# Kernel tuning notes

Measured on AMD Instinct MI355X. Metric: run time of the kernel, lower is better.

The kernel has to match this reference:

```python
import jax, jax.numpy as jnp
import numpy as np

MAX_DIST = 5
D_PE = 16
NUM_ENTITIES = 50000
NUM_EDGES = 800000
NUM_ANCHOR_TRIPLES = 32
MAX_SOURCES = 2 * NUM_ANCHOR_TRIPLES  # upper bound on unique anchor entities


def setup_inputs() -> dict:
    key = jax.random.key(0)
    k1, k2, k3, k4 = jax.random.split(key, 4)
    h_ids = jax.random.randint(k1, (NUM_EDGES,), 0, NUM_ENTITIES)
    t_ids = jax.random.randint(k2, (NUM_EDGES,), 0, NUM_ENTITIES)
    anchor_triple_indices = jax.random.randint(k3, (NUM_ANCHOR_TRIPLES,), 0, NUM_EDGES)
    dist_embed = jax.random.normal(k4, (MAX_DIST + 1, D_PE), dtype=jnp.float32)
    return {
        "h_ids": h_ids,
        "t_ids": t_ids,
        "anchor_triple_indices": anchor_triple_indices,
        "num_entities": NUM_ENTITIES,
        "dist_embed": dist_embed,
    }


def _bfs_mean_counts(h_ids, t_ids, anchor_triple_indices, num_entities):
    """Returns [num_entities, MAX_DIST+1] mean one-hot distance counts over anchors."""
    # unique anchor entities, padded with -1 to a static size (torch.unique equivalent)
    anchor_ents = jnp.concatenate([h_ids[anchor_triple_indices], t_ids[anchor_triple_indices]])
    sources = jnp.unique(anchor_ents, size=MAX_SOURCES, fill_value=-1)  # [K], sorted
    valid = sources >= 0                                                # [K]
    src = jnp.where(valid, sources, 0)
    K = src.shape[0]
    col = jnp.arange(K)

    # symmetric adjacency as edge list (duplicates are harmless: only >0 is tested)
    edge_src = jnp.concatenate([h_ids, t_ids])  # [2E]
    edge_dst = jnp.concatenate([t_ids, h_ids])  # [2E]

    frontier = jnp.zeros((num_entities, K), jnp.float32).at[src, col].set(1.0)
    visited = jnp.zeros((num_entities, K), bool).at[src, col].set(True)
    dist = jnp.full((num_entities, K), MAX_DIST, jnp.int32).at[src, col].set(0)

    for depth in range(1, MAX_DIST + 1):  # fixed small hop count
        # sparse adj @ frontier == scatter-add of gathered frontier rows
        new_frontier = jax.ops.segment_sum(frontier[edge_src], edge_dst, num_segments=num_entities)
        newly = (new_frontier > 0) & ~visited
        dist = jnp.where(newly, depth, dist)
        visited = visited | newly
        frontier = newly.astype(jnp.float32)

    # masked mean over valid anchor sources, expressed as distance-count histogram
    w = valid.astype(jnp.float32)
    n_valid = jnp.maximum(w.sum(), 1.0)
    onehot = jax.nn.one_hot(dist, MAX_DIST + 1, dtype=jnp.float32)  # [N, K, D+1]
    counts = jnp.einsum('nkd,k->nd', onehot, w) / n_valid           # [N, D+1]
    return counts


def reference(h_ids, t_ids, anchor_triple_indices, num_entities, dist_embed):
    counts = _bfs_mean_counts(h_ids, t_ids, anchor_triple_indices, num_entities)
    # mean over sources of embed(dist) == counts @ embedding table
    return counts @ dist_embed  # [num_entities, d_pe]
```

## Files before the change

### kernel.cpp

```cpp
#include <hip/hip_runtime.h>
#include <hip/hip_bf16.h>

typedef unsigned long long u64;
typedef unsigned int u32;
typedef unsigned short u16;

#define MAXD 5
#define BSH  6
#define BN   64
#define NW   1024
#define NTH  256
#define CAPG 2816
#define HEMPTY 0xFFFFFFFFu


__global__ __launch_bounds__(NTH) void chunk_sort(
    const int* __restrict__ h, const int* __restrict__ t, int E, int CE, int CAPC,
    int NB, u32* __restrict__ recs, u16* __restrict__ segtab,
    const int* __restrict__ anchor, int A,
    u64* __restrict__ NFg, u32* __restrict__ srcPack, int* __restrict__ nvalid) {
    extern __shared__ u32 sh[];
    u32* buf   = sh;
    u32* offs  = buf + CAPC;
    u32* cur   = offs + NB;
    u32* hsKey = cur + NB;
    u32* hsBit = hsKey + 128;
    u32* waveSum = hsBit + 128;
    int tid = threadIdx.x, c = blockIdx.x;
    int lane = tid & 63, w = tid >> 6;
    int lo = c * CE, hi = min(E, lo + CE);
    int ne = hi - lo;
    int nrec = 2 * ne;

    for (int i = tid; i < NB; i += NTH) cur[i] = 0u;
    if (tid < 128) hsKey[tid] = HEMPTY;
    __syncthreads();

    if (tid < 64) {
        int K = 2 * A;
        int a_ = (tid < K) ? anchor[(tid < A) ? tid : (tid - A)] : 0;
        int my = (tid < K) ? ((tid < A) ? h[a_] : t[a_]) : -1;
        bool uniq = (tid < K);
        for (int j = 0; j < 64; ++j) {
            int o = __shfl(my, j, 64);
            if (j < tid && o == my) uniq = false;
        }
        u64 mask = __ballot(uniq);
        if (c == 0 && tid == 0) *nvalid = (int)__popcll(mask);
        if (uniq) {
            u32 slot = ((u32)my * 2654435761u) >> 25;
            while (atomicCAS(&hsKey[slot], HEMPTY, (u32)my) != HEMPTY)
                slot = (slot + 1) & 127u;
            hsBit[slot] = (u32)tid;
        }
        if (c == 0)
            srcPack[tid] = uniq ? (((u32)my << BSH) | (u32)tid) : HEMPTY;
    }

    for (int i = tid; i < ne; i += NTH) {
        u32 uu = (u32)h[lo + i], vv = (u32)t[lo + i];
        atomicAdd(&cur[vv >> BSH], 1u);
        atomicAdd(&cur[uu >> BSH], 1u);
    }
    __syncthreads();

    {
        u32 i0 = (u32)tid * 4;
        u32 aa[4];
#pragma unroll
        for (int k = 0; k < 4; ++k) {
            u32 i = i0 + k;
            aa[k] = (i < (u32)NB) ? cur[i] : 0u;
        }
        u32 sum = aa[0] + aa[1] + aa[2] + aa[3];
        u32 p = sum;
#pragma unroll
        for (int d = 1; d < 64; d <<= 1) {
            u32 x = (u32)__shfl_up((int)p, d, 64);
            if (lane >= d) p += x;
        }
        u32 excl = p - sum;
        if (lane == 63) waveSum[w] = p;
        __syncthreads();
        u32 woff = 0;
        for (int k = 0; k < w; ++k) woff += waveSum[k];
        u32 o0 = woff + excl;
        u32 oo[4] = {o0, o0 + aa[0], o0 + aa[0] + aa[1],
                     o0 + aa[0] + aa[1] + aa[2]};
#pragma unroll
        for (int k = 0; k < 4; ++k) {
            u32 i = i0 + k;
            if (i < (u32)NB) {
                offs[i] = oo[k];
                segtab[c * (NB + 1) + i] = (u16)oo[k];
                cur[i] = 0u;
            }
        }
        if (tid == 0) segtab[c * (NB + 1) + NB] = (u16)nrec;
    }
    __syncthreads();

    auto srcMask = [&](u32 src) -> u64 {
        u32 slot = (src * 2654435761u) >> 25;
        while (true) {
            u32 k = hsKey[slot];
            if (k == src) return 1ull << hsBit[slot];
            if (k == HEMPTY) return 0ull;
            slot = (slot + 1) & 127u;
        }
    };

    for (int i = tid; i < ne; i += NTH) {
        u32 uu = (u32)h[lo + i], vv = (u32)t[lo + i];
        u32 b1 = vv >> BSH;
        buf[offs[b1] + atomicAdd(&cur[b1], 1u)] = (uu << BSH) | (vv & (BN - 1));
        u32 b2 = uu >> BSH;
        buf[offs[b2] + atomicAdd(&cur[b2], 1u)] = (vv << BSH) | (uu & (BN - 1));
        if (uu != vv) {
            u64 m1 = srcMask(uu);
            if (m1) atomicOr(&NFg[vv], m1);
            u64 m2 = srcMask(vv);
            if (m2) atomicOr(&NFg[uu], m2);
        }
    }
    __syncthreads();
    for (int i = tid; i < nrec; i += NTH) recs[c * CAPC + i] = buf[i];
}

__global__ __launch_bounds__(NTH) void level12_merge(
    const u32* __restrict__ recs, const u16* __restrict__ segtab, int CAPC, int NB,
    const u32* __restrict__ srcPack, const u64* __restrict__ NFg,
    u64* __restrict__ F2, u64* __restrict__ V, u64* __restrict__ CNT,
    u32* __restrict__ recs2, u32* __restrict__ bucketCnt, int N) {
    __shared__ u16 s0a[NW];
    __shared__ u32 loff[NW + 1];
    __shared__ u32 waveSum[4];
    __shared__ u32 buf[CAPG];
    __shared__ u64 NF[BN];
    __shared__ u32 srcL[64];
    int b = blockIdx.x, tid = threadIdx.x;
    int lane = tid & 63, w = tid >> 6;
    if (tid < BN) NF[tid] = 0ull;
    if (tid < 64) srcL[tid] = srcPack[tid];

    u32 c0 = (u32)tid * 4;
    u32 aa[4], ll[4];
#pragma unroll
    for (int k = 0; k < 4; ++k) {
        u32 c = c0 + k;
        u32 a = segtab[c * (NB + 1) + b];
        u32 e = segtab[c * (NB + 1) + b + 1];
        s0a[c] = (u16)a;
        aa[k] = a;
        ll[k] = e - a;
    }
    u32 sum = ll[0] + ll[1] + ll[2] + ll[3];
    u32 p = sum;
#pragma unroll
    for (int d = 1; d < 64; d <<= 1) {
        u32 x = (u32)__shfl_up((int)p, d, 64);
        if (lane >= d) p += x;
    }
    u32 excl = p - sum;
    if (lane == 63) waveSum[w] = p;
    __syncthreads();
    u32 woff = 0;
    for (int k = 0; k < w; ++k) woff += waveSum[k];
    u32 base = woff + excl;
    loff[c0]     = base;
    loff[c0 + 1] = base + ll[0];
    loff[c0 + 2] = base + ll[0] + ll[1];
    loff[c0 + 3] = base + ll[0] + ll[1] + ll[2];
    if (tid == NTH - 1) loff[NW] = base + sum;
    (void)aa;
    __syncthreads();

    u32 T = min(loff[NW], (u32)CAPG);

    u32 per = (T + NTH - 1) / NTH;
    u32 j0 = min((u32)tid * per, T), j1 = min(j0 + per, T);
    if (j0 < j1) {
        int c = 0;
#pragma unroll
        for (int step = 512; step >= 1; step >>= 1)
            if (c + step <= NW - 1 && loff[c + step] <= j0) c += step;
        for (u32 j = j0; j < j1; ++j) {
            while (loff[c + 1] <= j) ++c;
            buf[j] = recs[(u32)c * CAPC + (u32)s0a[c] + (j - loff[c])];
        }
    }
    __syncthreads();

    u32 o0 = (u32)b * CAPG;
    u32 r = tid;
    for (; r + 3u * NTH < T; r += 4u * NTH) {
        u32 r0 = buf[r],           r1 = buf[r + NTH];
        u32 r2 = buf[r + 2 * NTH], r3 = buf[r + 3 * NTH];
        recs2[o0 + r] = r0;
        recs2[o0 + r + NTH] = r1;
        recs2[o0 + r + 2 * NTH] = r2;
        recs2[o0 + r + 3 * NTH] = r3;
        u64 f0 = NFg[r0 >> BSH], f1 = NFg[r1 >> BSH];
        u64 f2 = NFg[r2 >> BSH], f3 = NFg[r3 >> BSH];
        if (f0) atomicOr(&NF[r0 & (BN - 1)], f0);
        if (f1) atomicOr(&NF[r1 & (BN - 1)], f1);
        if (f2) atomicOr(&NF[r2 & (BN - 1)], f2);
        if (f3) atomicOr(&NF[r3 & (BN - 1)], f3);
    }
    for (; r < T; r += NTH) {
        u32 r0 = buf[r];
        recs2[o0 + r] = r0;
        u64 f0 = NFg[r0 >> BSH];
        if (f0) atomicOr(&NF[r0 & (BN - 1)], f0);
    }
    __syncthreads();
    if (tid == 0) bucketCnt[b] = T;
    if (tid < BN) {
        int n = b * BN + tid;
        if (n < N) {
            u64 srcbit = 0ull;
            for (int k = 0; k < 64; ++k) {
                u32 pk = srcL[k];
                if (pk != HEMPTY && (int)(pk >> BSH) == n)
                    srcbit |= 1ull << (pk & (BN - 1));
            }
            u64 nf1 = NFg[n];
            u64 v1 = srcbit | nf1;
            u64 newly2 = NF[tid] & ~v1;
            V[n] = v1 | newly2;
            F2[n] = newly2;
            CNT[n] = (srcbit ? 1ull : 0ull)
                   | ((u64)__popcll(nf1) << 8)
                   | ((u64)__popcll(newly2) << 16);
        }
    }
}

__global__ __launch_bounds__(NTH) void level3(
    const u32* __restrict__ recs2, const u32* __restrict__ bucketCnt,
    const u64* __restrict__ Fin, u64* __restrict__ Fout,
    u64* __restrict__ V, u64* __restrict__ CNT, int N) {
    __shared__ u64 NF[BN];
    int b = blockIdx.x, tid = threadIdx.x;
    u32 o0 = (u32)b * CAPG;
    u32 cnt = bucketCnt[b];
    if (tid < BN) NF[tid] = 0ull;
    __syncthreads();
    u32 r = tid;
    for (; r + 3u * NTH < cnt; r += 4u * NTH) {
        u32 c0 = recs2[o0 + r],           c1 = recs2[o0 + r + NTH];
        u32 c2 = recs2[o0 + r + 2 * NTH], c3 = recs2[o0 + r + 3 * NTH];
        u64 f0 = Fin[c0 >> BSH], f1 = Fin[c1 >> BSH];
        u64 f2 = Fin[c2 >> BSH], f3 = Fin[c3 >> BSH];
        if (f0) atomicOr(&NF[c0 & (BN - 1)], f0);
        if (f1) atomicOr(&NF[c1 & (BN - 1)], f1);
        if (f2) atomicOr(&NF[c2 & (BN - 1)], f2);
        if (f3) atomicOr(&NF[c3 & (BN - 1)], f3);
    }
    for (; r < cnt; r += NTH) {
        u32 c0 = recs2[o0 + r];
        u64 f0 = Fin[c0 >> BSH];
        if (f0) atomicOr(&NF[c0 & (BN - 1)], f0);
    }
    __syncthreads();
    if (tid < BN) {
        int n = b * BN + tid;
        if (n < N) {
            u64 vis = V[n];
            u64 newly = NF[tid] & ~vis;
            Fout[n] = newly;
            if (newly) {
                V[n] = vis | newly;
                CNT[n] += (u64)__popcll(newly) << 24;
            }
        }
    }
}

__global__ __launch_bounds__(NTH) void level4_fin(
    const u32* __restrict__ recs2, const u32* __restrict__ bucketCnt,
    const u64* __restrict__ Fin, const u64* __restrict__ V,
    const u64* __restrict__ CNT, const int* __restrict__ nvalid,
    const float* __restrict__ embed, float* __restrict__ out, int N) {
    __shared__ u64 NF[BN];
    int b = blockIdx.x, tid = threadIdx.x;
    u32 o0 = (u32)b * CAPG;
    u32 cnt = bucketCnt[b];
    if (tid < BN) NF[tid] = 0ull;
    __syncthreads();
    u32 r = tid;
    for (; r + 3u * NTH < cnt; r += 4u * NTH) {
        u32 c0 = recs2[o0 + r],           c1 = recs2[o0 + r + NTH];
        u32 c2 = recs2[o0 + r + 2 * NTH], c3 = recs2[o0 + r + 3 * NTH];
        u64 f0 = Fin[c0 >> BSH], f1 = Fin[c1 >> BSH];
        u64 f2 = Fin[c2 >> BSH], f3 = Fin[c3 >> BSH];
        if (f0) atomicOr(&NF[c0 & (BN - 1)], f0);
        if (f1) atomicOr(&NF[c1 & (BN - 1)], f1);
        if (f2) atomicOr(&NF[c2 & (BN - 1)], f2);
        if (f3) atomicOr(&NF[c3 & (BN - 1)], f3);
    }
    for (; r < cnt; r += NTH) {
        u32 c0 = recs2[o0 + r];
        u64 f0 = Fin[c0 >> BSH];
        if (f0) atomicOr(&NF[c0 & (BN - 1)], f0);
    }
    __syncthreads();
    int nl = tid >> 2, q = tid & 3;
    int n = b * BN + nl;
    if (n >= N) return;
    u64 vis = V[n];
    int c4 = __popcll(NF[nl] & ~vis);
    u64 c = CNT[n];
    int nv = *nvalid;
    float inv = 1.0f / (float)(nv > 0 ? nv : 1);
    float cd[MAXD + 1];
    int total = c4;
#pragma unroll
    for (int d = 0; d < 4; ++d) {
        int x = (int)((c >> (8 * d)) & 0xffull);
        total += x;
        cd[d] = (float)x;
    }
    cd[4] = (float)c4;
    cd[5] = (float)(nv - total);

    const float4* e4 = (const float4*)embed;
    float4 acc = {0.f, 0.f, 0.f, 0.f};
#pragma unroll
    for (int d = 0; d <= MAXD; ++d) {
        float4 e = e4[d * 4 + q];
        acc.x += cd[d] * e.x; acc.y += cd[d] * e.y;
        acc.z += cd[d] * e.z; acc.w += cd[d] * e.w;
    }
    acc.x *= inv; acc.y *= inv; acc.z *= inv; acc.w *= inv;
    ((float4*)(out + (size_t)n * 16))[q] = acc;
}

extern "C" void kernel_launch(void* const* d_in, const int* in_sizes, int n_in,
                              void* d_out, int out_size, void* d_ws, size_t ws_size,
                              hipStream_t stream) {
    const int*   h      = (const int*)d_in[0];
    const int*   t      = (const int*)d_in[1];
    const int*   anchor = (const int*)d_in[2];
    const float* embed  = (const float*)d_in[4];
    float*       out    = (float*)d_out;

    int E = in_sizes[0];
    int A = in_sizes[2];
    int D = in_sizes[4] / (MAXD + 1);
    int N = out_size / D;
    int NB = (N + BN - 1) >> BSH;
    int CE = (E + NW - 1) / NW;
    int CAPC = 2 * CE;
    (void)D;

    u64* NFg = (u64*)d_ws;
    u64* V   = NFg + N;
    u64* CNT = V + N;
    u64* F2  = CNT + N;
    u64* F3  = F2 + N;
    u32* srcPack   = (u32*)(F3 + N);
    int* nvalid    = (int*)(srcPack + 64);
    u32* bucketCnt = (u32*)(nvalid + 1);
    u32* recs      = bucketCnt + NB;
    u16* segtab    = (u16*)(recs + (size_t)NW * CAPC);
    u32* recs2     = (u32*)(segtab + (size_t)NW * (NB + 1));

    hipMemsetAsync(NFg, 0, (size_t)N * 8, stream);

    size_t shmem = (size_t)(CAPC + 2 * NB + 260) * sizeof(u32);
    chunk_sort<<<NW, NTH, shmem, stream>>>(h, t, E, CE, CAPC, NB, recs, segtab,
                                           anchor, A, NFg, srcPack, nvalid);

    level12_merge<<<NB, NTH, 0, stream>>>(recs, segtab, CAPC, NB, srcPack, NFg,
                                          F2, V, CNT, recs2, bucketCnt, N);
    level3<<<NB, NTH, 0, stream>>>(recs2, bucketCnt, F2, F3, V, CNT, N);
    level4_fin<<<NB, NTH, 0, stream>>>(recs2, bucketCnt, F3, V, CNT,
                                       nvalid, embed, out, N);
}
```

Baseline: 135.2 us.

## Fuse BFS stages into one persistent kernel with grid-wide barriers

Merges the chunk sort, level-1/2 merge, level-3 and final level-4 kernels into a single launch. Stages are separated by a software grid barrier built on an atomic counter, and the NFg memset is moved into the kernel. Each block keeps its gathered bucket records, visited bits and counts in shared memory across levels, so the recs2, V, CNT and bucketCnt global round trips go away. The chunk count now equals the bucket count so all blocks can be co-resident. This risks deadlock if not every block is resident, and the barrier spin adds its own latency.

```diff
diff --git a/kernel.cpp b/kernel.cpp
--- a/kernel.cpp
+++ b/kernel.cpp
@@ -1,5 +1,4 @@
 #include <hip/hip_runtime.h>
-#include <hip/hip_bf16.h>
 
 typedef unsigned long long u64;
 typedef unsigned int u32;
@@ -8,71 +7,207 @@
 #define MAXD 5
 #define BSH  6
 #define BN   64
-#define NW   1024
 #define NTH  256
 #define CAPG 2816
+#define MAXC 1024
 #define HEMPTY 0xFFFFFFFFu
 
 
-__global__ __launch_bounds__(NTH) void chunk_sort(
+__device__ __forceinline__ void gbar(u32* bar, u32 target) {
+    __syncthreads();
+    if (threadIdx.x == 0) {
+        __threadfence();
+        atomicAdd(bar, 1u);
+        while (__hip_atomic_load(bar, __ATOMIC_RELAXED,
+                                 __HIP_MEMORY_SCOPE_AGENT) < target)
+            __builtin_amdgcn_s_sleep(2);
+        __threadfence();
+    }
+    __syncthreads();
+}
+
+__global__ __launch_bounds__(NTH, 4) void fused(
     const int* __restrict__ h, const int* __restrict__ t, int E, int CE, int CAPC,
     int NB, u32* __restrict__ recs, u16* __restrict__ segtab,
     const int* __restrict__ anchor, int A,
-    u64* __restrict__ NFg, u32* __restrict__ srcPack, int* __restrict__ nvalid) {
+    u64* __restrict__ NFg, u32* __restrict__ srcPack, int* __restrict__ nvalid,
+    u32* __restrict__ bar,
+    u64* __restrict__ F2g, u64* __restrict__ F3g,
+    const float* __restrict__ embed, float* __restrict__ out, int N) {
     extern __shared__ u32 sh[];
-    u32* buf   = sh;
-    u32* offs  = buf + CAPC;
-    u32* cur   = offs + NB;
-    u32* hsKey = cur + NB;
-    u32* hsBit = hsKey + 128;
-    u32* waveSum = hsBit + 128;
-    int tid = threadIdx.x, c = blockIdx.x;
-    int lane = tid & 63, w = tid >> 6;
-    int lo = c * CE, hi = min(E, lo + CE);
-    int ne = hi - lo;
-    int nrec = 2 * ne;
-
-    for (int i = tid; i < NB; i += NTH) cur[i] = 0u;
-    if (tid < 128) hsKey[tid] = HEMPTY;
-    __syncthreads();
-
-    if (tid < 64) {
-        int K = 2 * A;
-        int a_ = (tid < K) ? anchor[(tid < A) ? tid : (tid - A)] : 0;
-        int my = (tid < K) ? ((tid < A) ? h[a_] : t[a_]) : -1;
-        bool uniq = (tid < K);
-        for (int j = 0; j < 64; ++j) {
-            int o = __shfl(my, j, 64);
-            if (j < tid && o == my) uniq = false;
-        }
-        u64 mask = __ballot(uniq);
-        if (c == 0 && tid == 0) *nvalid = (int)__popcll(mask);
-        if (uniq) {
-            u32 slot = ((u32)my * 2654435761u) >> 25;
-            while (atomicCAS(&hsKey[slot], HEMPTY, (u32)my) != HEMPTY)
+    const int tid = threadIdx.x;
+    const int b = blockIdx.x;
+    const int lane = tid & 63, w = tid >> 6;
+    const u32 nb = (u32)gridDim.x;
+
+    u32* buf2 = sh;
+    u64* NF   = (u64*)(sh + CAPG);
+    u64* Vl   = NF + BN;
+    u64* CNTl = Vl + BN;
+    u32* scr  = (u32*)(CNTl + BN);
+    u16* s0a  = (u16*)scr;
+    u32* loff = scr + MAXC / 2;
+    u32* wS2  = loff + MAXC + 1;
+    u32* srcL = wS2 + 4;
+
+    { int i = b * NTH + tid; if (i < N) NFg[i] = 0ull; }
+    gbar(bar, nb);
+
+    {
+        u32* cbuf  = sh;
+        u32* offs  = cbuf + CAPC;
+        u32* cur   = offs + NB;
+        u32* hsKey = cur + NB;
+        u32* hsBit = hsKey + 128;
+        u32* wS    = hsBit + 128;
+        int lo = b * CE, hi = min(E, lo + CE);
+        int ne = hi - lo, nrec = 2 * ne;
+
+        for (int i = tid; i < NB; i += NTH) cur[i] = 0u;
+        if (tid < 128) hsKey[tid] = HEMPTY;
+        __syncthreads();
+
+        if (tid < 64) {
+            int K = 2 * A;
+            int a_ = (tid < K) ? anchor[(tid < A) ? tid : (tid - A)] : 0;
+            int my = (tid < K) ? ((tid < A) ? h[a_] : t[a_]) : -1;
+            bool uniq = (tid < K);
+            for (int j = 0; j < 64; ++j) {
+                int o = __shfl(my, j, 64);
+                if (j < tid && o == my) uniq = false;
+            }
+            u64 mask = __ballot(uniq);
+            if (b == 0 && tid == 0) *nvalid = (int)__popcll(mask);
+            if (uniq) {
+                u32 slot = ((u32)my * 2654435761u) >> 25;
+                while (atomicCAS(&hsKey[slot], HEMPTY, (u32)my) != HEMPTY)
+                    slot = (slot + 1) & 127u;
+                hsBit[slot] = (u32)tid;
+            }
+            if (b == 0)
+                srcPack[tid] = uniq ? (((u32)my << BSH) | (u32)tid) : HEMPTY;
+        }
+
+        u32 eu[4], ev[4];
+#pragma unroll
+        for (int k = 0; k < 4; ++k) {
+            int i = tid + k * NTH;
+            u32 uu = 0u, vv = 0u;
+            if (i < ne) {
+                uu = (u32)h[lo + i]; vv = (u32)t[lo + i];
+                atomicAdd(&cur[vv >> BSH], 1u);
+                atomicAdd(&cur[uu >> BSH], 1u);
+            }
+            eu[k] = uu; ev[k] = vv;
+        }
+        for (int i = tid + 4 * NTH; i < ne; i += NTH) {
+            u32 uu = (u32)h[lo + i], vv = (u32)t[lo + i];
+            atomicAdd(&cur[vv >> BSH], 1u);
+            atomicAdd(&cur[uu >> BSH], 1u);
+        }
+        __syncthreads();
+
+        {
+            u32 i0 = (u32)tid * 4;
+            u32 aa[4];
+#pragma unroll
+            for (int k = 0; k < 4; ++k) {
+                u32 i = i0 + k;
+                aa[k] = (i < (u32)NB) ? cur[i] : 0u;
+            }
+            u32 sum = aa[0] + aa[1] + aa[2] + aa[3];
+            u32 p = sum;
+#pragma unroll
+            for (int d = 1; d < 64; d <<= 1) {
+                u32 x = (u32)__shfl_up((int)p, d, 64);
+                if (lane >= d) p += x;
+            }
+            u32 excl = p - sum;
+            if (lane == 63) wS[w] = p;
+            __syncthreads();
+            u32 woff = 0;
+            for (int k = 0; k < w; ++k) woff += wS[k];
+            u32 o0 = woff + excl;
+            u32 oo[4] = {o0, o0 + aa[0], o0 + aa[0] + aa[1],
+                         o0 + aa[0] + aa[1] + aa[2]};
+#pragma unroll
+            for (int k = 0; k < 4; ++k) {
+                u32 i = i0 + k;
+                if (i < (u32)NB) {
+                    offs[i] = oo[k];
+                    segtab[b * (NB + 1) + i] = (u16)oo[k];
+                    cur[i] = 0u;
+                }
+            }
+            if (tid == 0) segtab[b * (NB + 1) + NB] = (u16)nrec;
+        }
+        __syncthreads();
+
+        auto srcMask = [&](u32 src) -> u64 {
+            u32 slot = (src * 2654435761u) >> 25;
+            while (true) {
+                u32 k = hsKey[slot];
+                if (k == src) return 1ull << hsBit[slot];
+                if (k == HEMPTY) return 0ull;
                 slot = (slot + 1) & 127u;
-            hsBit[slot] = (u32)tid;
-        }
-        if (c == 0)
-            srcPack[tid] = uniq ? (((u32)my << BSH) | (u32)tid) : HEMPTY;
+            }
+        };
+
+#pragma unroll
+        for (int k = 0; k < 4; ++k) {
+            int i = tid + k * NTH;
+            if (i < ne) {
+                u32 uu = eu[k], vv = ev[k];
+                u32 b1 = vv >> BSH;
+                cbuf[offs[b1] + atomicAdd(&cur[b1], 1u)] = (uu << BSH) | (vv & (BN - 1));
+                u32 b2 = uu >> BSH;
+                cbuf[offs[b2] + atomicAdd(&cur[b2], 1u)] = (vv << BSH) | (uu & (BN - 1));
+                if (uu != vv) {
+                    u64 m1 = srcMask(uu);
+                    if (m1) atomicOr(&NFg[vv], m1);
+                    u64 m2 = srcMask(vv);
+                    if (m2) atomicOr(&NFg[uu], m2);
+                }
+            }
+        }
+        for (int i = tid + 4 * NTH; i < ne; i += NTH) {
+            u32 uu = (u32)h[lo + i], vv = (u32)t[lo + i];
+            u32 b1 = vv >> BSH;
+            cbuf[offs[b1] + atomicAdd(&cur[b1], 1u)] = (uu << BSH) | (vv & (BN - 1));
+            u32 b2 = uu >> BSH;
+            cbuf[offs[b2] + atomicAdd(&cur[b2], 1u)] = (vv << BSH) | (uu & (BN - 1));
+            if (uu != vv) {
+                u64 m1 = srcMask(uu);
+                if (m1) atomicOr(&NFg[vv], m1);
+                u64 m2 = srcMask(vv);
+                if (m2) atomicOr(&NFg[uu], m2);
+            }
+        }
+        __syncthreads();
+        for (int i = tid; i < nrec; i += NTH) recs[b * CAPC + i] = cbuf[i];
     }
-
-    for (int i = tid; i < ne; i += NTH) {
-        u32 uu = (u32)h[lo + i], vv = (u32)t[lo + i];
-        atomicAdd(&cur[vv >> BSH], 1u);
-        atomicAdd(&cur[uu >> BSH], 1u);
-    }
-    __syncthreads();
-
+    gbar(bar, 2 * nb);
+
+    u32 T;
     {
-        u32 i0 = (u32)tid * 4;
-        u32 aa[4];
+        if (tid < BN) NF[tid] = 0ull;
+        if (tid < 64) srcL[tid] = srcPack[tid];
+
+        u32 c0 = (u32)tid * 4;
+        u32 ll[4];
 #pragma unroll
         for (int k = 0; k < 4; ++k) {
-            u32 i = i0 + k;
-            aa[k] = (i < (u32)NB) ? cur[i] : 0u;
-        }
-        u32 sum = aa[0] + aa[1] + aa[2] + aa[3];
+            u32 c = c0 + k;
+            u32 l_ = 0u;
+            if (c < (u32)NB) {
+                u32 a = segtab[c * (NB + 1) + b];
+                u32 e = segtab[c * (NB + 1) + b + 1];
+                s0a[c] = (u16)a;
+                l_ = e - a;
+            }
+            ll[k] = l_;
+        }
+        u32 sum = ll[0] + ll[1] + ll[2] + ll[3];
         u32 p = sum;
 #pragma unroll
         for (int d = 1; d < 64; d <<= 1) {
@@ -80,260 +215,149 @@
             if (lane >= d) p += x;
         }
         u32 excl = p - sum;
-        if (lane == 63) waveSum[w] = p;
+        if (lane == 63) wS2[w] = p;
         __syncthreads();
         u32 woff = 0;
-        for (int k = 0; k < w; ++k) woff += waveSum[k];
-        u32 o0 = woff + excl;
-        u32 oo[4] = {o0, o0 + aa[0], o0 + aa[0] + aa[1],
-                     o0 + aa[0] + aa[1] + aa[2]};
-#pragma unroll
-        for (int k = 0; k < 4; ++k) {
-            u32 i = i0 + k;
-            if (i < (u32)NB) {
-                offs[i] = oo[k];
-                segtab[c * (NB + 1) + i] = (u16)oo[k];
-                cur[i] = 0u;
-            }
-        }
-        if (tid == 0) segtab[c * (NB + 1) + NB] = (u16)nrec;
+        for (int k = 0; k < w; ++k) woff += wS2[k];
+        u32 base = woff + excl;
+        loff[c0]     = base;
+        loff[c0 + 1] = base + ll[0];
+        loff[c0 + 2] = base + ll[0] + ll[1];
+        loff[c0 + 3] = base + ll[0] + ll[1] + ll[2];
+        if (tid == NTH - 1) loff[MAXC] = base + sum;
+        __syncthreads();
+        T = min(loff[MAXC], (u32)CAPG);
+
+        u32 per = (T + NTH - 1) / NTH;
+        u32 j0 = min((u32)tid * per, T), j1 = min(j0 + per, T);
+        if (j0 < j1) {
+            int c = 0;
+#pragma unroll
+            for (int step = 512; step >= 1; step >>= 1)
+                if (c + step <= MAXC - 1 && loff[c + step] <= j0) c += step;
+            for (u32 j = j0; j < j1; ++j) {
+                while (loff[c + 1] <= j) ++c;
+                buf2[j] = recs[(u32)c * CAPC + (u32)s0a[c] + (j - loff[c])];
+            }
+        }
+        __syncthreads();
+
+        u32 r = tid;
+        for (; r + 3u * NTH < T; r += 4u * NTH) {
+            u32 r0 = buf2[r],           r1 = buf2[r + NTH];
+            u32 r2 = buf2[r + 2 * NTH], r3 = buf2[r + 3 * NTH];
+            u64 f0 = NFg[r0 >> BSH], f1 = NFg[r1 >> BSH];
+            u64 f2 = NFg[r2 >> BSH], f3 = NFg[r3 >> BSH];
+            if (f0) atomicOr(&NF[r0 & (BN - 1)], f0);
+            if (f1) atomicOr(&NF[r1 & (BN - 1)], f1);
+            if (f2) atomicOr(&NF[r2 & (BN - 1)], f2);
+            if (f3) atomicOr(&NF[r3 & (BN - 1)], f3);
+        }
+        for (; r < T; r += NTH) {
+            u32 r0 = buf2[r];
+            u64 f0 = NFg[r0 >> BSH];
+            if (f0) atomicOr(&NF[r0 & (BN - 1)], f0);
+        }
+        __syncthreads();
+        if (tid < BN) {
+            int n = b * BN + tid;
+            u64 v2 = 0ull, cnt = 0ull;
+            if (n < N) {
+                u64 srcbit = 0ull;
+                for (int k = 0; k < 64; ++k) {
+                    u32 pk = srcL[k];
+                    if (pk != HEMPTY && (int)(pk >> BSH) == n)
+                        srcbit |= 1ull << (pk & (BN - 1));
+                }
+                u64 nf1 = NFg[n];
+                u64 v1 = srcbit | nf1;
+                u64 newly2 = NF[tid] & ~v1;
+                v2 = v1 | newly2;
+                F2g[n] = newly2;
+                cnt = (srcbit ? 1ull : 0ull)
+                    | ((u64)__popcll(nf1) << 8)
+                    | ((u64)__popcll(newly2) << 16);
+            }
+            Vl[tid] = v2;
+            CNTl[tid] = cnt;
+        }
     }
-    __syncthreads();
-
-    auto srcMask = [&](u32 src) -> u64 {
-        u32 slot = (src * 2654435761u) >> 25;
-        while (true) {
-            u32 k = hsKey[slot];
-            if (k == src) return 1ull << hsBit[slot];
-            if (k == HEMPTY) return 0ull;
-            slot = (slot + 1) & 127u;
+    gbar(bar, 3 * nb);
+
+    auto depth_pass = [&](const u64* __restrict__ Fin) {
+        u32 r = tid;
+        for (; r + 3u * NTH < T; r += 4u * NTH) {
+            u32 r0 = buf2[r],           r1 = buf2[r + NTH];
+            u32 r2 = buf2[r + 2 * NTH], r3 = buf2[r + 3 * NTH];
+            u64 f0 = Fin[r0 >> BSH], f1 = Fin[r1 >> BSH];
+            u64 f2 = Fin[r2 >> BSH], f3 = Fin[r3 >> BSH];
+            if (f0) atomicOr(&NF[r0 & (BN - 1)], f0);
+            if (f1) atomicOr(&NF[r1 & (BN - 1)], f1);
+            if (f2) atomicOr(&NF[r2 & (BN - 1)], f2);
+            if (f3) atomicOr(&NF[r3 & (BN - 1)], f3);
+        }
+        for (; r < T; r += NTH) {
+            u32 r0 = buf2[r];
+            u64 f0 = Fin[r0 >> BSH];
+            if (f0) atomicOr(&NF[r0 & (BN - 1)], f0);
         }
     };
 
-    for (int i = tid; i < ne; i += NTH) {
-        u32 uu = (u32)h[lo + i], vv = (u32)t[lo + i];
-        u32 b1 = vv >> BSH;
-        buf[offs[b1] + atomicAdd(&cur[b1], 1u)] = (uu << BSH) | (vv & (BN - 1));
-        u32 b2 = uu >> BSH;
-        buf[offs[b2] + atomicAdd(&cur[b2], 1u)] = (vv << BSH) | (uu & (BN - 1));
-        if (uu != vv) {
-            u64 m1 = srcMask(uu);
-            if (m1) atomicOr(&NFg[vv], m1);
-            u64 m2 = srcMask(vv);
-            if (m2) atomicOr(&NFg[uu], m2);
+    {
+        if (tid < BN) NF[tid] = 0ull;
+        __syncthreads();
+        depth_pass(F2g);
+        __syncthreads();
+        if (tid < BN) {
+            int n = b * BN + tid;
+            if (n < N) {
+                u64 vis = Vl[tid];
+                u64 newly = NF[tid] & ~vis;
+                F3g[n] = newly;
+                if (newly) {
+                    Vl[tid] = vis | newly;
+                    CNTl[tid] += (u64)__popcll(newly) << 24;
+                }
+            }
         }
     }
-    __syncthreads();
-    for (int i = tid; i < nrec; i += NTH) recs[c * CAPC + i] = buf[i];
-}
-
-__global__ __launch_bounds__(NTH) void level12_merge(
-    const u32* __restrict__ recs, const u16* __restrict__ segtab, int CAPC, int NB,
-    const u32* __restrict__ srcPack, const u64* __restrict__ NFg,
-    u64* __restrict__ F2, u64* __restrict__ V, u64* __restrict__ CNT,
-    u32* __restrict__ recs2, u32* __restrict__ bucketCnt, int N) {
-    __shared__ u16 s0a[NW];
-    __shared__ u32 loff[NW + 1];
-    __shared__ u32 waveSum[4];
-    __shared__ u32 buf[CAPG];
-    __shared__ u64 NF[BN];
-    __shared__ u32 srcL[64];
-    int b = blockIdx.x, tid = threadIdx.x;
-    int lane = tid & 63, w = tid >> 6;
-    if (tid < BN) NF[tid] = 0ull;
-    if (tid < 64) srcL[tid] = srcPack[tid];
-
-    u32 c0 = (u32)tid * 4;
-    u32 aa[4], ll[4];
-#pragma unroll
-    for (int k = 0; k < 4; ++k) {
-        u32 c = c0 + k;
-        u32 a = segtab[c * (NB + 1) + b];
-        u32 e = segtab[c * (NB + 1) + b + 1];
-        s0a[c] = (u16)a;
-        aa[k] = a;
-        ll[k] = e - a;
+    gbar(bar, 4 * nb);
+
+    {
+        if (tid < BN) NF[tid] = 0ull;
+        __syncthreads();
+        depth_pass(F3g);
+        __syncthreads();
+        int nl = tid >> 2, q = tid & 3;
+        int n = b * BN + nl;
+        if (n >= N) return;
+        u64 vis = Vl[nl];
+        int c4 = __popcll(NF[nl] & ~vis);
+        u64 c = CNTl[nl];
+        int nv = *nvalid;
+        float inv = 1.0f / (float)(nv > 0 ? nv : 1);
+        float cd[MAXD + 1];
+        int total = c4;
+#pragma unroll
+        for (int d = 0; d < 4; ++d) {
+            int x = (int)((c >> (8 * d)) & 0xffull);
+            total += x;
+            cd[d] = (float)x;
+        }
+        cd[4] = (float)c4;
+        cd[5] = (float)(nv - total);
+
+        const float4* e4 = (const float4*)embed;
+        float4 acc = {0.f, 0.f, 0.f, 0.f};
+#pragma unroll
+        for (int d = 0; d <= MAXD; ++d) {
+            float4 e = e4[d * 4 + q];
+            acc.x += cd[d] * e.x; acc.y += cd[d] * e.y;
+            acc.z += cd[d] * e.z; acc.w += cd[d] * e.w;
+        }
+        acc.x *= inv; acc.y *= inv; acc.z *= inv; acc.w *= inv;
+        ((float4*)(out + (size_t)n * 16))[q] = acc;
     }
-    u32 sum = ll[0] + ll[1] + ll[2] + ll[3];
-    u32 p = sum;
-#pragma unroll
-    for (int d = 1; d < 64; d <<= 1) {
-        u32 x = (u32)__shfl_up((int)p, d, 64);
-        if (lane >= d) p += x;
-    }
-    u32 excl = p - sum;
-    if (lane == 63) waveSum[w] = p;
-    __syncthreads();
-    u32 woff = 0;
-    for (int k = 0; k < w; ++k) woff += waveSum[k];
-    u32 base = woff + excl;
-    loff[c0]     = base;
-    loff[c0 + 1] = base + ll[0];
-    loff[c0 + 2] = base + ll[0] + ll[1];
-    loff[c0 + 3] = base + ll[0] + ll[1] + ll[2];
-    if (tid == NTH - 1) loff[NW] = base + sum;
-    (void)aa;
-    __syncthreads();
-
-    u32 T = min(loff[NW], (u32)CAPG);
-
-    u32 per = (T + NTH - 1) / NTH;
-    u32 j0 = min((u32)tid * per, T), j1 = min(j0 + per, T);
-    if (j0 < j1) {
-        int c = 0;
-#pragma unroll
-        for (int step = 512; step >= 1; step >>= 1)
-            if (c + step <= NW - 1 && loff[c + step] <= j0) c += step;
-        for (u32 j = j0; j < j1; ++j) {
-            while (loff[c + 1] <= j) ++c;
-            buf[j] = recs[(u32)c * CAPC + (u32)s0a[c] + (j - loff[c])];
-        }
-    }
-    __syncthreads();
-
-    u32 o0 = (u32)b * CAPG;
-    u32 r = tid;
-    for (; r + 3u * NTH < T; r += 4u * NTH) {
-        u32 r0 = buf[r],           r1 = buf[r + NTH];
-        u32 r2 = buf[r + 2 * NTH], r3 = buf[r + 3 * NTH];
-        recs2[o0 + r] = r0;
-        recs2[o0 + r + NTH] = r1;
-        recs2[o0 + r + 2 * NTH] = r2;
-        recs2[o0 + r + 3 * NTH] = r3;
-        u64 f0 = NFg[r0 >> BSH], f1 = NFg[r1 >> BSH];
-        u64 f2 = NFg[r2 >> BSH], f3 = NFg[r3 >> BSH];
-        if (f0) atomicOr(&NF[r0 & (BN - 1)], f0);
-        if (f1) atomicOr(&NF[r1 & (BN - 1)], f1);
-        if (f2) atomicOr(&NF[r2 & (BN - 1)], f2);
-        if (f3) atomicOr(&NF[r3 & (BN - 1)], f3);
-    }
-    for (; r < T; r += NTH) {
-        u32 r0 = buf[r];
-        recs2[o0 + r] = r0;
-        u64 f0 = NFg[r0 >> BSH];
-        if (f0) atomicOr(&NF[r0 & (BN - 1)], f0);
-    }
-    __syncthreads();
-    if (tid == 0) bucketCnt[b] = T;
-    if (tid < BN) {
-        int n = b * BN + tid;
-        if (n < N) {
-            u64 srcbit = 0ull;
-            for (int k = 0; k < 64; ++k) {
-                u32 pk = srcL[k];
-                if (pk != HEMPTY && (int)(pk >> BSH) == n)
-                    srcbit |= 1ull << (pk & (BN - 1));
-            }
-            u64 nf1 = NFg[n];
-            u64 v1 = srcbit | nf1;
-            u64 newly2 = NF[tid] & ~v1;
-            V[n] = v1 | newly2;
-            F2[n] = newly2;
-            CNT[n] = (srcbit ? 1ull : 0ull)
-                   | ((u64)__popcll(nf1) << 8)
-                   | ((u64)__popcll(newly2) << 16);
-        }
-    }
-}
-
-__global__ __launch_bounds__(NTH) void level3(
-    const u32* __restrict__ recs2, const u32* __restrict__ bucketCnt,
-    const u64* __restrict__ Fin, u64* __restrict__ Fout,
-    u64* __restrict__ V, u64* __restrict__ CNT, int N) {
-    __shared__ u64 NF[BN];
-    int b = blockIdx.x, tid = threadIdx.x;
-    u32 o0 = (u32)b * CAPG;
-    u32 cnt = bucketCnt[b];
-    if (tid < BN) NF[tid] = 0ull;
-    __syncthreads();
-    u32 r = tid;
-    for (; r + 3u * NTH < cnt; r += 4u * NTH) {
-        u32 c0 = recs2[o0 + r],           c1 = recs2[o0 + r + NTH];
-        u32 c2 = recs2[o0 + r + 2 * NTH], c3 = recs2[o0 + r + 3 * NTH];
-        u64 f0 = Fin[c0 >> BSH], f1 = Fin[c1 >> BSH];
-        u64 f2 = Fin[c2 >> BSH], f3 = Fin[c3 >> BSH];
-        if (f0) atomicOr(&NF[c0 & (BN - 1)], f0);
-        if (f1) atomicOr(&NF[c1 & (BN - 1)], f1);
-        if (f2) atomicOr(&NF[c2 & (BN - 1)], f2);
-        if (f3) atomicOr(&NF[c3 & (BN - 1)], f3);
-    }
-    for (; r < cnt; r += NTH) {
-        u32 c0 = recs2[o0 + r];
-        u64 f0 = Fin[c0 >> BSH];
-        if (f0) atomicOr(&NF[c0 & (BN - 1)], f0);
-    }
-    __syncthreads();
-    if (tid < BN) {
-        int n = b * BN + tid;
-        if (n < N) {
-            u64 vis = V[n];
-            u64 newly = NF[tid] & ~vis;
-            Fout[n] = newly;
-            if (newly) {
-                V[n] = vis | newly;
-                CNT[n] += (u64)__popcll(newly) << 24;
-            }
-        }
-    }
-}
-
-__global__ __launch_bounds__(NTH) void level4_fin(
-    const u32* __restrict__ recs2, const u32* __restrict__ bucketCnt,
-    const u64* __restrict__ Fin, const u64* __restrict__ V,
-    const u64* __restrict__ CNT, const int* __restrict__ nvalid,
-    const float* __restrict__ embed, float* __restrict__ out, int N) {
-    __shared__ u64 NF[BN];
-    int b = blockIdx.x, tid = threadIdx.x;
-    u32 o0 = (u32)b * CAPG;
-    u32 cnt = bucketCnt[b];
-    if (tid < BN) NF[tid] = 0ull;
-    __syncthreads();
-    u32 r = tid;
-    for (; r + 3u * NTH < cnt; r += 4u * NTH) {
-        u32 c0 = recs2[o0 + r],           c1 = recs2[o0 + r + NTH];
-        u32 c2 = recs2[o0 + r + 2 * NTH], c3 = recs2[o0 + r + 3 * NTH];
-        u64 f0 = Fin[c0 >> BSH], f1 = Fin[c1 >> BSH];
-        u64 f2 = Fin[c2 >> BSH], f3 = Fin[c3 >> BSH];
-        if (f0) atomicOr(&NF[c0 & (BN - 1)], f0);
-        if (f1) atomicOr(&NF[c1 & (BN - 1)], f1);
-        if (f2) atomicOr(&NF[c2 & (BN - 1)], f2);
-        if (f3) atomicOr(&NF[c3 & (BN - 1)], f3);
-    }
-    for (; r < cnt; r += NTH) {
-        u32 c0 = recs2[o0 + r];
-        u64 f0 = Fin[c0 >> BSH];
-        if (f0) atomicOr(&NF[c0 & (BN - 1)], f0);
-    }
-    __syncthreads();
-    int nl = tid >> 2, q = tid & 3;
-    int n = b * BN + nl;
-    if (n >= N) return;
-    u64 vis = V[n];
-    int c4 = __popcll(NF[nl] & ~vis);
-    u64 c = CNT[n];
-    int nv = *nvalid;
-    float inv = 1.0f / (float)(nv > 0 ? nv : 1);
-    float cd[MAXD + 1];
-    int total = c4;
-#pragma unroll
-    for (int d = 0; d < 4; ++d) {
-        int x = (int)((c >> (8 * d)) & 0xffull);
-        total += x;
-        cd[d] = (float)x;
-    }
-    cd[4] = (float)c4;
-    cd[5] = (float)(nv - total);
-
-    const float4* e4 = (const float4*)embed;
-    float4 acc = {0.f, 0.f, 0.f, 0.f};
-#pragma unroll
-    for (int d = 0; d <= MAXD; ++d) {
-        float4 e = e4[d * 4 + q];
-        acc.x += cd[d] * e.x; acc.y += cd[d] * e.y;
-        acc.z += cd[d] * e.z; acc.w += cd[d] * e.w;
-    }
-    acc.x *= inv; acc.y *= inv; acc.z *= inv; acc.w *= inv;
-    ((float4*)(out + (size_t)n * 16))[q] = acc;
 }
 
 extern "C" void kernel_launch(void* const* d_in, const int* in_sizes, int n_in,
@@ -350,31 +374,27 @@
     int D = in_sizes[4] / (MAXD + 1);
     int N = out_size / D;
     int NB = (N + BN - 1) >> BSH;
-    int CE = (E + NW - 1) / NW;
+    int CE = (E + NB - 1) / NB;
     int CAPC = 2 * CE;
     (void)D;
 
-    u64* NFg = (u64*)d_ws;
-    u64* V   = NFg + N;
-    u64* CNT = V + N;
-    u64* F2  = CNT + N;
-    u64* F3  = F2 + N;
-    u32* srcPack   = (u32*)(F3 + N);
-    int* nvalid    = (int*)(srcPack + 64);
-    u32* bucketCnt = (u32*)(nvalid + 1);
-    u32* recs      = bucketCnt + NB;
-    u16* segtab    = (u16*)(recs + (size_t)NW * CAPC);
-    u32* recs2     = (u32*)(segtab + (size_t)NW * (NB + 1));
-
-    hipMemsetAsync(NFg, 0, (size_t)N * 8, stream);
-
-    size_t shmem = (size_t)(CAPC + 2 * NB + 260) * sizeof(u32);
-    chunk_sort<<<NW, NTH, shmem, stream>>>(h, t, E, CE, CAPC, NB, recs, segtab,
-                                           anchor, A, NFg, srcPack, nvalid);
-
-    level12_merge<<<NB, NTH, 0, stream>>>(recs, segtab, CAPC, NB, srcPack, NFg,
-                                          F2, V, CNT, recs2, bucketCnt, N);
-    level3<<<NB, NTH, 0, stream>>>(recs2, bucketCnt, F2, F3, V, CNT, N);
-    level4_fin<<<NB, NTH, 0, stream>>>(recs2, bucketCnt, F3, V, CNT,
-                                       nvalid, embed, out, N);
+    u64* NFg     = (u64*)d_ws;
+    u64* F2      = NFg + N;
+    u64* F3      = F2 + N;
+    u32* srcPack = (u32*)(F3 + N);
+    int* nvalid  = (int*)(srcPack + 64);
+    u32* bar     = (u32*)(nvalid + 1);
+    u32* recs    = (u32*)(srcPack + 72);
+    u16* segtab  = (u16*)(recs + (size_t)NB * CAPC);
+
+    hipMemsetAsync(bar, 0, 4, stream);
+
+    size_t shA = (size_t)(CAPC + 2 * NB + 260) * sizeof(u32);
+    size_t shB = (size_t)CAPG * 4 + 3 * BN * 8
+               + (size_t)MAXC * 2 + (size_t)(MAXC + 1 + 4 + 64) * 4;
+    size_t shmem = (((shA > shB ? shA : shB) + 255) / 256) * 256;
+
+    fused<<<NB, NTH, shmem, stream>>>(h, t, E, CE, CAPC, NB, recs, segtab,
+                                      anchor, A, NFg, srcPack, nvalid, bar,
+                                      F2, F3, embed, out, N);
 }
```

Result: slower. 429.1 us (+217.5%).

## Replace two-pass chunk sort and merge with direct global atomic bucket scatter

Applied to the files above, without the earlier changes.

Drops the per-chunk shared-memory counting sort and the segment-table merge kernel. Each edge now claims its slot in a per-bucket global array through a global atomic counter and writes its record straight into place. The depth-2 kernel then reads those buckets directly. This removes one full write and read of the intermediate records plus the prefix-scan and merge work, in exchange for heavy global atomic contention across about 782 bucket counters and a nondeterministic record order within each bucket.

```diff
diff --git a/kernel.cpp b/kernel.cpp
--- a/kernel.cpp
+++ b/kernel.cpp
@@ -1,38 +1,23 @@
 #include <hip/hip_runtime.h>
-#include <hip/hip_bf16.h>
 
 typedef unsigned long long u64;
 typedef unsigned int u32;
-typedef unsigned short u16;
 
 #define MAXD 5
 #define BSH  6
 #define BN   64
-#define NW   1024
 #define NTH  256
 #define CAPG 2816
 #define HEMPTY 0xFFFFFFFFu
 
 
-__global__ __launch_bounds__(NTH) void chunk_sort(
-    const int* __restrict__ h, const int* __restrict__ t, int E, int CE, int CAPC,
-    int NB, u32* __restrict__ recs, u16* __restrict__ segtab,
+__global__ __launch_bounds__(NTH) void build_scatter(
+    const int* __restrict__ h, const int* __restrict__ t, int E,
     const int* __restrict__ anchor, int A,
-    u64* __restrict__ NFg, u32* __restrict__ srcPack, int* __restrict__ nvalid) {
-    extern __shared__ u32 sh[];
-    u32* buf   = sh;
-    u32* offs  = buf + CAPC;
-    u32* cur   = offs + NB;
-    u32* hsKey = cur + NB;
-    u32* hsBit = hsKey + 128;
-    u32* waveSum = hsBit + 128;
-    int tid = threadIdx.x, c = blockIdx.x;
-    int lane = tid & 63, w = tid >> 6;
-    int lo = c * CE, hi = min(E, lo + CE);
-    int ne = hi - lo;
-    int nrec = 2 * ne;
-
-    for (int i = tid; i < NB; i += NTH) cur[i] = 0u;
+    u64* __restrict__ NFg, u32* __restrict__ srcPack, int* __restrict__ nvalid,
+    u32* __restrict__ bucketCur, u32* __restrict__ recs2) {
+    __shared__ u32 hsKey[128], hsBit[128];
+    int tid = threadIdx.x, b = blockIdx.x;
     if (tid < 128) hsKey[tid] = HEMPTY;
     __syncthreads();
 
@@ -46,57 +31,15 @@
             if (j < tid && o == my) uniq = false;
         }
         u64 mask = __ballot(uniq);
-        if (c == 0 && tid == 0) *nvalid = (int)__popcll(mask);
+        if (b == 0 && tid == 0) *nvalid = (int)__popcll(mask);
         if (uniq) {
             u32 slot = ((u32)my * 2654435761u) >> 25;
             while (atomicCAS(&hsKey[slot], HEMPTY, (u32)my) != HEMPTY)
                 slot = (slot + 1) & 127u;
             hsBit[slot] = (u32)tid;
         }
-        if (c == 0)
+        if (b == 0)
             srcPack[tid] = uniq ? (((u32)my << BSH) | (u32)tid) : HEMPTY;
-    }
-
-    for (int i = tid; i < ne; i += NTH) {
-        u32 uu = (u32)h[lo + i], vv = (u32)t[lo + i];
-        atomicAdd(&cur[vv >> BSH], 1u);
-        atomicAdd(&cur[uu >> BSH], 1u);
-    }
-    __syncthreads();
-
-    {
-        u32 i0 = (u32)tid * 4;
-        u32 aa[4];
-#pragma unroll
-        for (int k = 0; k < 4; ++k) {
-            u32 i = i0 + k;
-            aa[k] = (i < (u32)NB) ? cur[i] : 0u;
-        }
-        u32 sum = aa[0] + aa[1] + aa[2] + aa[3];
-        u32 p = sum;
-#pragma unroll
-        for (int d = 1; d < 64; d <<= 1) {
-            u32 x = (u32)__shfl_up((int)p, d, 64);
-            if (lane >= d) p += x;
-        }
-        u32 excl = p - sum;
-        if (lane == 63) waveSum[w] = p;
-        __syncthreads();
-        u32 woff = 0;
-        for (int k = 0; k < w; ++k) woff += waveSum[k];
-        u32 o0 = woff + excl;
-        u32 oo[4] = {o0, o0 + aa[0], o0 + aa[0] + aa[1],
-                     o0 + aa[0] + aa[1] + aa[2]};
-#pragma unroll
-        for (int k = 0; k < 4; ++k) {
-            u32 i = i0 + k;
-            if (i < (u32)NB) {
-                offs[i] = oo[k];
-                segtab[c * (NB + 1) + i] = (u16)oo[k];
-                cur[i] = 0u;
-            }
-        }
-        if (tid == 0) segtab[c * (NB + 1) + NB] = (u16)nrec;
     }
     __syncthreads();
 
@@ -110,111 +53,62 @@
         }
     };
 
-    for (int i = tid; i < ne; i += NTH) {
-        u32 uu = (u32)h[lo + i], vv = (u32)t[lo + i];
-        u32 b1 = vv >> BSH;
-        buf[offs[b1] + atomicAdd(&cur[b1], 1u)] = (uu << BSH) | (vv & (BN - 1));
-        u32 b2 = uu >> BSH;
-        buf[offs[b2] + atomicAdd(&cur[b2], 1u)] = (vv << BSH) | (uu & (BN - 1));
-        if (uu != vv) {
-            u64 m1 = srcMask(uu);
-            if (m1) atomicOr(&NFg[vv], m1);
-            u64 m2 = srcMask(vv);
-            if (m2) atomicOr(&NFg[uu], m2);
-        }
-    }
-    __syncthreads();
-    for (int i = tid; i < nrec; i += NTH) recs[c * CAPC + i] = buf[i];
-}
-
-__global__ __launch_bounds__(NTH) void level12_merge(
-    const u32* __restrict__ recs, const u16* __restrict__ segtab, int CAPC, int NB,
+    int base = b * (4 * NTH);
+#pragma unroll
+    for (int k = 0; k < 4; ++k) {
+        int i = base + k * NTH + tid;
+        if (i < E) {
+            u32 uu = (u32)h[i], vv = (u32)t[i];
+            u32 b1 = vv >> BSH, b2 = uu >> BSH;
+            u32 p1 = atomicAdd(&bucketCur[b1], 1u);
+            u32 p2 = atomicAdd(&bucketCur[b2], 1u);
+            if (p1 < CAPG)
+                __hip_atomic_store(&recs2[(u32)b1 * CAPG + p1],
+                                   (uu << BSH) | (vv & (BN - 1)),
+                                   __ATOMIC_RELAXED, __HIP_MEMORY_SCOPE_AGENT);
+            if (p2 < CAPG)
+                __hip_atomic_store(&recs2[(u32)b2 * CAPG + p2],
+                                   (vv << BSH) | (uu & (BN - 1)),
+                                   __ATOMIC_RELAXED, __HIP_MEMORY_SCOPE_AGENT);
+            if (uu != vv) {
+                u64 m1 = srcMask(uu);
+                if (m1) atomicOr(&NFg[vv], m1);
+                u64 m2 = srcMask(vv);
+                if (m2) atomicOr(&NFg[uu], m2);
+            }
+        }
+    }
+}
+
+__global__ __launch_bounds__(NTH) void depth2_init(
+    const u32* __restrict__ recs2, const u32* __restrict__ bucketCur,
     const u32* __restrict__ srcPack, const u64* __restrict__ NFg,
-    u64* __restrict__ F2, u64* __restrict__ V, u64* __restrict__ CNT,
-    u32* __restrict__ recs2, u32* __restrict__ bucketCnt, int N) {
-    __shared__ u16 s0a[NW];
-    __shared__ u32 loff[NW + 1];
-    __shared__ u32 waveSum[4];
-    __shared__ u32 buf[CAPG];
+    u64* __restrict__ F2, u64* __restrict__ V, u64* __restrict__ CNT, int N) {
     __shared__ u64 NF[BN];
     __shared__ u32 srcL[64];
     int b = blockIdx.x, tid = threadIdx.x;
-    int lane = tid & 63, w = tid >> 6;
     if (tid < BN) NF[tid] = 0ull;
     if (tid < 64) srcL[tid] = srcPack[tid];
-
-    u32 c0 = (u32)tid * 4;
-    u32 aa[4], ll[4];
-#pragma unroll
-    for (int k = 0; k < 4; ++k) {
-        u32 c = c0 + k;
-        u32 a = segtab[c * (NB + 1) + b];
-        u32 e = segtab[c * (NB + 1) + b + 1];
-        s0a[c] = (u16)a;
-        aa[k] = a;
-        ll[k] = e - a;
-    }
-    u32 sum = ll[0] + ll[1] + ll[2] + ll[3];
-    u32 p = sum;
-#pragma unroll
-    for (int d = 1; d < 64; d <<= 1) {
-        u32 x = (u32)__shfl_up((int)p, d, 64);
-        if (lane >= d) p += x;
-    }
-    u32 excl = p - sum;
-    if (lane == 63) waveSum[w] = p;
-    __syncthreads();
-    u32 woff = 0;
-    for (int k = 0; k < w; ++k) woff += waveSum[k];
-    u32 base = woff + excl;
-    loff[c0]     = base;
-    loff[c0 + 1] = base + ll[0];
-    loff[c0 + 2] = base + ll[0] + ll[1];
-    loff[c0 + 3] = base + ll[0] + ll[1] + ll[2];
-    if (tid == NTH - 1) loff[NW] = base + sum;
-    (void)aa;
-    __syncthreads();
-
-    u32 T = min(loff[NW], (u32)CAPG);
-
-    u32 per = (T + NTH - 1) / NTH;
-    u32 j0 = min((u32)tid * per, T), j1 = min(j0 + per, T);
-    if (j0 < j1) {
-        int c = 0;
-#pragma unroll
-        for (int step = 512; step >= 1; step >>= 1)
-            if (c + step <= NW - 1 && loff[c + step] <= j0) c += step;
-        for (u32 j = j0; j < j1; ++j) {
-            while (loff[c + 1] <= j) ++c;
-            buf[j] = recs[(u32)c * CAPC + (u32)s0a[c] + (j - loff[c])];
-        }
-    }
-    __syncthreads();
-
+    __syncthreads();
+    u32 cnt = min(bucketCur[b], (u32)CAPG);
     u32 o0 = (u32)b * CAPG;
     u32 r = tid;
-    for (; r + 3u * NTH < T; r += 4u * NTH) {
-        u32 r0 = buf[r],           r1 = buf[r + NTH];
-        u32 r2 = buf[r + 2 * NTH], r3 = buf[r + 3 * NTH];
-        recs2[o0 + r] = r0;
-        recs2[o0 + r + NTH] = r1;
-        recs2[o0 + r + 2 * NTH] = r2;
-        recs2[o0 + r + 3 * NTH] = r3;
-        u64 f0 = NFg[r0 >> BSH], f1 = NFg[r1 >> BSH];
-        u64 f2 = NFg[r2 >> BSH], f3 = NFg[r3 >> BSH];
-        if (f0) atomicOr(&NF[r0 & (BN - 1)], f0);
-        if (f1) atomicOr(&NF[r1 & (BN - 1)], f1);
-        if (f2) atomicOr(&NF[r2 & (BN - 1)], f2);
-        if (f3) atomicOr(&NF[r3 & (BN - 1)], f3);
-    }
-    for (; r < T; r += NTH) {
-        u32 r0 = buf[r];
-        recs2[o0 + r] = r0;
-        u64 f0 = NFg[r0 >> BSH];
-        if (f0) atomicOr(&NF[r0 & (BN - 1)], f0);
-    }
-    __syncthreads();
-    if (tid == 0) bucketCnt[b] = T;
+    for (; r + 3u * NTH < cnt; r += 4u * NTH) {
+        u32 c0 = recs2[o0 + r],           c1 = recs2[o0 + r + NTH];
+        u32 c2 = recs2[o0 + r + 2 * NTH], c3 = recs2[o0 + r + 3 * NTH];
+        u64 f0 = NFg[c0 >> BSH], f1 = NFg[c1 >> BSH];
+        u64 f2 = NFg[c2 >> BSH], f3 = NFg[c3 >> BSH];
+        if (f0) atomicOr(&NF[c0 & (BN - 1)], f0);
+        if (f1) atomicOr(&NF[c1 & (BN - 1)], f1);
+        if (f2) atomicOr(&NF[c2 & (BN - 1)], f2);
+        if (f3) atomicOr(&NF[c3 & (BN - 1)], f3);
+    }
+    for (; r < cnt; r += NTH) {
+        u32 c0 = recs2[o0 + r];
+        u64 f0 = NFg[c0 >> BSH];
+        if (f0) atomicOr(&NF[c0 & (BN - 1)], f0);
+    }
+    __syncthreads();
     if (tid < BN) {
         int n = b * BN + tid;
         if (n < N) {
@@ -237,13 +131,13 @@
 }
 
 __global__ __launch_bounds__(NTH) void level3(
-    const u32* __restrict__ recs2, const u32* __restrict__ bucketCnt,
+    const u32* __restrict__ recs2, const u32* __restrict__ bucketCur,
     const u64* __restrict__ Fin, u64* __restrict__ Fout,
     u64* __restrict__ V, u64* __restrict__ CNT, int N) {
     __shared__ u64 NF[BN];
     int b = blockIdx.x, tid = threadIdx.x;
     u32 o0 = (u32)b * CAPG;
-    u32 cnt = bucketCnt[b];
+    u32 cnt = min(bucketCur[b], (u32)CAPG);
     if (tid < BN) NF[tid] = 0ull;
     __syncthreads();
     u32 r = tid;
@@ -278,14 +172,14 @@
 }
 
 __global__ __launch_bounds__(NTH) void level4_fin(
-    const u32* __restrict__ recs2, const u32* __restrict__ bucketCnt,
+    const u32* __restrict__ recs2, const u32* __restrict__ bucketCur,
     const u64* __restrict__ Fin, const u64* __restrict__ V,
     const u64* __restrict__ CNT, const int* __restrict__ nvalid,
     const float* __restrict__ embed, float* __restrict__ out, int N) {
     __shared__ u64 NF[BN];
     int b = blockIdx.x, tid = threadIdx.x;
     u32 o0 = (u32)b * CAPG;
-    u32 cnt = bucketCnt[b];
+    u32 cnt = min(bucketCur[b], (u32)CAPG);
     if (tid < BN) NF[tid] = 0ull;
     __syncthreads();
     u32 r = tid;
@@ -350,31 +244,29 @@
     int D = in_sizes[4] / (MAXD + 1);
     int N = out_size / D;
     int NB = (N + BN - 1) >> BSH;
-    int CE = (E + NW - 1) / NW;
-    int CAPC = 2 * CE;
+    int NB1 = (E + 4 * NTH - 1) / (4 * NTH);
     (void)D;
 
-    u64* NFg = (u64*)d_ws;
-    u64* V   = NFg + N;
+    u64* NFg       = (u64*)d_ws;
+    u32* bucketCur = (u32*)(NFg + N);
+    size_t zb = (size_t)N * 8 + (size_t)NB * 4;
+    char* p  = (char*)d_ws + ((zb + 15) & ~(size_t)15);
+    u64* V   = (u64*)p;
     u64* CNT = V + N;
     u64* F2  = CNT + N;
     u64* F3  = F2 + N;
-    u32* srcPack   = (u32*)(F3 + N);
-    int* nvalid    = (int*)(srcPack + 64);
-    u32* bucketCnt = (u32*)(nvalid + 1);
-    u32* recs      = bucketCnt + NB;
-    u16* segtab    = (u16*)(recs + (size_t)NW * CAPC);
-    u32* recs2     = (u32*)(segtab + (size_t)NW * (NB + 1));
-
-    hipMemsetAsync(NFg, 0, (size_t)N * 8, stream);
-
-    size_t shmem = (size_t)(CAPC + 2 * NB + 260) * sizeof(u32);
-    chunk_sort<<<NW, NTH, shmem, stream>>>(h, t, E, CE, CAPC, NB, recs, segtab,
-                                           anchor, A, NFg, srcPack, nvalid);
-
-    level12_merge<<<NB, NTH, 0, stream>>>(recs, segtab, CAPC, NB, srcPack, NFg,
-                                          F2, V, CNT, recs2, bucketCnt, N);
-    level3<<<NB, NTH, 0, stream>>>(recs2, bucketCnt, F2, F3, V, CNT, N);
-    level4_fin<<<NB, NTH, 0, stream>>>(recs2, bucketCnt, F3, V, CNT,
+    u32* srcPack = (u32*)(F3 + N);
+    int* nvalid  = (int*)(srcPack + 64);
+    u32* recs2   = (u32*)(srcPack + 72);
+
+    hipMemsetAsync(NFg, 0, zb, stream);
+
+    build_scatter<<<NB1, NTH, 0, stream>>>(h, t, E, anchor, A,
+                                           NFg, srcPack, nvalid,
+                                           bucketCur, recs2);
+    depth2_init<<<NB, NTH, 0, stream>>>(recs2, bucketCur, srcPack, NFg,
+                                        F2, V, CNT, N);
+    level3<<<NB, NTH, 0, stream>>>(recs2, bucketCur, F2, F3, V, CNT, N);
+    level4_fin<<<NB, NTH, 0, stream>>>(recs2, bucketCur, F3, V, CNT,
                                        nvalid, embed, out, N);
 }
```

New measurement: 484.8 us. 3.59x slower.
